# Kernel optimization log

Measured on AMD Instinct MI355X. Metric: run time of the kernel, lower is better.

## Reference

```python
import jax, jax.numpy as jnp
import numpy as np

N_VERTICES = 500000
N_EDGES = 32000000


def setup_inputs() -> dict:
    key = jax.random.key(0)
    k1, k2, k3 = jax.random.split(key, 3)
    vertex_attr = jax.random.normal(k1, (N_VERTICES, 2), dtype=jnp.float32)
    edgeij_pair = jax.random.randint(k2, (2, N_EDGES), 0, N_VERTICES, dtype=jnp.int32)
    edge_attr = jax.random.normal(k3, (N_EDGES, 1), dtype=jnp.float32)
    g = jnp.zeros((1, 1), dtype=jnp.float32)
    batch = jnp.zeros((N_VERTICES,), dtype=jnp.int32)
    return {"vertex_attr": vertex_attr, "edgeij_pair": edgeij_pair,
            "edge_attr": edge_attr, "g": g, "batch": batch}


def reference(vertex_attr, edgeij_pair, edge_attr, g, batch):
    # y_i = second column of vertex_attr, kept as [N,1]
    y_i = vertex_attr[:, 1:2]
    n_vertices = vertex_attr.shape[0]
    # edge-to-vertex scatter-sum aggregation: cbar_i = sum_{j in N(i)} c_ij
    # destination vertex index is row 0 of edgeij_pair
    cbar_i = jax.ops.segment_sum(edge_attr, edgeij_pair[0], num_segments=n_vertices)  # [N,1]
    return jnp.concatenate([cbar_i, y_i], axis=1)  # [N,2]
```

## Files before the change

### kernel.cpp

```cpp
#include <hip/hip_runtime.h>


__global__ void vertex_init_kernel(const float* __restrict__ vattr,
                                   float* __restrict__ out, int n) {
    int i = blockIdx.x * blockDim.x + threadIdx.x;
    if (i < n) {
        float2 va = reinterpret_cast<const float2*>(vattr)[i];
        float2 o = make_float2(0.0f, va.y);
        reinterpret_cast<float2*>(out)[i] = o;
    }
}

__global__ void edge_scatter_kernel(const int* __restrict__ eidx,
                                    const float* __restrict__ eattr,
                                    float* __restrict__ out, int ne4) {
    int tid = blockIdx.x * blockDim.x + threadIdx.x;
    int stride = gridDim.x * blockDim.x;
    for (int i = tid; i < ne4; i += stride) {
        int4   id = reinterpret_cast<const int4*>(eidx)[i];
        float4 v  = reinterpret_cast<const float4*>(eattr)[i];
        atomicAdd(&out[2 * id.x], v.x);
        atomicAdd(&out[2 * id.y], v.y);
        atomicAdd(&out[2 * id.z], v.z);
        atomicAdd(&out[2 * id.w], v.w);
    }
}

extern "C" void kernel_launch(void* const* d_in, const int* in_sizes, int n_in,
                              void* d_out, int out_size, void* d_ws, size_t ws_size,
                              hipStream_t stream) {
    const float* vattr = (const float*)d_in[0];
    const int*   eij   = (const int*)d_in[1];
    const float* eattr = (const float*)d_in[2];
    float* out = (float*)d_out;

    const int n_vertices = in_sizes[0] / 2;
    const int n_edges    = in_sizes[2];
    const int ne4        = n_edges / 4;

    {
        int block = 256;
        int grid = (n_vertices + block - 1) / block;
        vertex_init_kernel<<<grid, block, 0, stream>>>(vattr, out, n_vertices);
    }
    {
        int block = 256;
        int grid = 2048;
        edge_scatter_kernel<<<grid, block, 0, stream>>>(eij, eattr, out, ne4);
    }
}
```

Measured before the change: 1.838 ms.

## Privatize scatter accumulators per XCD with workgroup-scope atomics, then reduce copies

Each XCD, identified through the hardware XCC_ID register, accumulates edge values into its own zeroed copy of the vertex sums in workspace. The atomics use relaxed workgroup scope so they can resolve in that XCD's L2 instead of device-wide coherent memory. A final kernel sums the eight copies and writes the y column. This adds a memset and a reduction pass over 8 arrays, and correctness depends on the assumption that all waves on one XCD share an L2 and that scope-limited atomics are coherent there. Without enough workspace the old path runs.

```diff
diff --git a/kernel.cpp b/kernel.cpp
--- a/kernel.cpp
+++ b/kernel.cpp
@@ -1,19 +1,54 @@
 #include <hip/hip_runtime.h>
 
+
+#define GETREG_IMM(SZ, OFF, ID) ((((SZ)-1) << 11) | ((OFF) << 6) | (ID))
+#define HW_REG_XCC_ID 20
+
+constexpr int    kNumXcd     = 8;
+constexpr size_t kCopyStride = 512 * 1024;
+
+__global__ void edge_scatter_local(const int* __restrict__ eidx,
+                                   const float* __restrict__ eattr,
+                                   float* __restrict__ ws, int ne4) {
+    int xcc = __builtin_amdgcn_s_getreg(GETREG_IMM(32, 0, HW_REG_XCC_ID)) & (kNumXcd - 1);
+    float* mycopy = ws + (size_t)xcc * kCopyStride;
+    int tid = blockIdx.x * blockDim.x + threadIdx.x;
+    int stride = gridDim.x * blockDim.x;
+    for (int i = tid; i < ne4; i += stride) {
+        int4   id = reinterpret_cast<const int4*>(eidx)[i];
+        float4 v  = reinterpret_cast<const float4*>(eattr)[i];
+        __hip_atomic_fetch_add(&mycopy[id.x], v.x, __ATOMIC_RELAXED, __HIP_MEMORY_SCOPE_WORKGROUP);
+        __hip_atomic_fetch_add(&mycopy[id.y], v.y, __ATOMIC_RELAXED, __HIP_MEMORY_SCOPE_WORKGROUP);
+        __hip_atomic_fetch_add(&mycopy[id.z], v.z, __ATOMIC_RELAXED, __HIP_MEMORY_SCOPE_WORKGROUP);
+        __hip_atomic_fetch_add(&mycopy[id.w], v.w, __ATOMIC_RELAXED, __HIP_MEMORY_SCOPE_WORKGROUP);
+    }
+}
+
+__global__ void reduce_copies(const float* __restrict__ ws,
+                              const float* __restrict__ vattr,
+                              float* __restrict__ out, int n) {
+    int i = blockIdx.x * blockDim.x + threadIdx.x;
+    if (i < n) {
+        float s = 0.0f;
+        #pragma unroll
+        for (int x = 0; x < kNumXcd; ++x) s += ws[(size_t)x * kCopyStride + i];
+        float y = vattr[2 * i + 1];
+        reinterpret_cast<float2*>(out)[i] = make_float2(s, y);
+    }
+}
 
 __global__ void vertex_init_kernel(const float* __restrict__ vattr,
                                    float* __restrict__ out, int n) {
     int i = blockIdx.x * blockDim.x + threadIdx.x;
     if (i < n) {
         float2 va = reinterpret_cast<const float2*>(vattr)[i];
-        float2 o = make_float2(0.0f, va.y);
-        reinterpret_cast<float2*>(out)[i] = o;
+        reinterpret_cast<float2*>(out)[i] = make_float2(0.0f, va.y);
     }
 }
 
-__global__ void edge_scatter_kernel(const int* __restrict__ eidx,
-                                    const float* __restrict__ eattr,
-                                    float* __restrict__ out, int ne4) {
+__global__ void edge_scatter_agent(const int* __restrict__ eidx,
+                                   const float* __restrict__ eattr,
+                                   float* __restrict__ out, int ne4) {
     int tid = blockIdx.x * blockDim.x + threadIdx.x;
     int stride = gridDim.x * blockDim.x;
     for (int i = tid; i < ne4; i += stride) {
@@ -38,14 +73,31 @@
     const int n_edges    = in_sizes[2];
     const int ne4        = n_edges / 4;
 
-    {
-        int block = 256;
-        int grid = (n_vertices + block - 1) / block;
-        vertex_init_kernel<<<grid, block, 0, stream>>>(vattr, out, n_vertices);
-    }
-    {
-        int block = 256;
-        int grid = 2048;
-        edge_scatter_kernel<<<grid, block, 0, stream>>>(eij, eattr, out, ne4);
+    const size_t ws_needed = (size_t)kNumXcd * kCopyStride * sizeof(float);
+
+    if (ws_size >= ws_needed) {
+        float* ws = (float*)d_ws;
+        hipMemsetAsync(d_ws, 0, ws_needed, stream);
+        {
+            int block = 256;
+            int grid = 2048;
+            edge_scatter_local<<<grid, block, 0, stream>>>(eij, eattr, ws, ne4);
+        }
+        {
+            int block = 256;
+            int grid = (n_vertices + block - 1) / block;
+            reduce_copies<<<grid, block, 0, stream>>>(ws, vattr, out, n_vertices);
+        }
+    } else {
+        {
+            int block = 256;
+            int grid = (n_vertices + block - 1) / block;
+            vertex_init_kernel<<<grid, block, 0, stream>>>(vattr, out, n_vertices);
+        }
+        {
+            int block = 256;
+            int grid = 2048;
+            edge_scatter_agent<<<grid, block, 0, stream>>>(eij, eattr, out, ne4);
+        }
     }
 }
```

New measurement: 1.844 ms. No clear change (+0.3%).
